# Kernel tuning notes

Hardware: AMD Instinct MI355X
Metric: run time of the kernel (lower is better)

Reference implementation:

```python
import jax, jax.numpy as jnp
import numpy as np

B, S, E, H = 2, 2048, 1024, 16
DH = E // H
SCALE = 1.0 / float(np.sqrt(E))  # note: original scales by 1/sqrt(hidden_dim), not head_dim


def _icl_mask(s):
    # triu(diagonal=0) is masked (-inf): only strictly-past positions visible,
    # except (0,0) which is explicitly unmasked so row 0 attends to itself.
    m = jnp.triu(jnp.ones((s, s), dtype=bool), k=0)
    return m.at[0, 0].set(False)


def setup_inputs() -> dict:
    key = jax.random.key(0)
    ks = jax.random.split(key, 7)
    mk = lambda k, shp: jax.random.normal(k, shp, dtype=jnp.float32)
    return {
        "q": mk(ks[0], (B, S, E)),
        "k": mk(ks[1], (B, S, E)),
        "v": mk(ks[2], (B, S, E)),
        "Wq": mk(ks[3], (E, E)) * 0.02,
        "Wk": mk(ks[4], (E, E)) * 0.02,
        "Wv": mk(ks[5], (E, E)) * 0.02,
        "Wo": mk(ks[6], (E, E)) * 0.02,
    }


def reference(q, k, v, Wq, Wk, Wv, Wo):
    b, s, e = q.shape
    h, dh = H, e // H
    # projections (nn.Linear: x @ W.T), split heads -> [b, h, s, dh]
    qh = (q @ Wq.T).reshape(b, s, h, dh).transpose(0, 2, 1, 3)
    kh = (k @ Wk.T).reshape(b, s, h, dh).transpose(0, 2, 1, 3)
    vh = (v @ Wv.T).reshape(b, s, h, dh).transpose(0, 2, 1, 3)
    scores = jnp.einsum("bhsd,bhtd->bhst", qh, kh) * SCALE  # [b,h,s,s]
    scores = jnp.where(_icl_mask(s), -jnp.inf, scores)
    probs = jax.nn.softmax(scores, axis=-1)
    out = jnp.einsum("bhst,bhtd->bhsd", probs, vh)
    out = out.transpose(0, 2, 1, 3).reshape(b, s, e)
    return out @ Wo.T
```

## Files before the change

### kernel.cpp

```cpp
#include <hip/hip_runtime.h>
#include <hip/hip_bf16.h>

typedef unsigned short u16;
typedef unsigned int u32;
typedef __bf16 bf16x8 __attribute__((ext_vector_type(8)));
typedef float float4_ __attribute__((ext_vector_type(4)));

#define B_ 2
#define S_ 2048
#define E_ 1024
#define H_ 16
#define DH_ 64
#define M_ (B_*S_)
#define E2_ (E_*E_)
#define SCALE_ 0.03125f
#define LOG2E_ 1.4426950408889634f

__device__ __forceinline__ u16 f2bf(float f) {
    unsigned int x = __float_as_uint(f);
    x += 0x7fffu + ((x >> 16) & 1u);
    return (u16)(x >> 16);
}

template <typename T> struct raw8;
template <> struct raw8<float> { float4_ lo, hi; };
template <> struct raw8<u16>   { bf16x8 v; };

__device__ __forceinline__ raw8<float> ldr8(const float* p) {
    raw8<float> r; const float4_* q = (const float4_*)p; r.lo = q[0]; r.hi = q[1]; return r;
}
__device__ __forceinline__ raw8<u16> ldr8(const u16* p) {
    raw8<u16> r; r.v = *(const bf16x8*)p; return r;
}
__device__ __forceinline__ bf16x8 cvt8(const raw8<u16>& r) { return r.v; }
__device__ __forceinline__ bf16x8 cvt8(const raw8<float>& r) {
    union { bf16x8 v; __hip_bfloat162 h[4]; } u;
    u.h[0] = __float22bfloat162_rn(float2{r.lo[0], r.lo[1]});
    u.h[1] = __float22bfloat162_rn(float2{r.lo[2], r.lo[3]});
    u.h[2] = __float22bfloat162_rn(float2{r.hi[0], r.hi[1]});
    u.h[3] = __float22bfloat162_rn(float2{r.hi[2], r.hi[3]});
    return u.v;
}
__device__ __forceinline__ bf16x8 ld8(const u16* p) { return *(const bf16x8*)p; }

__device__ __forceinline__ void async16(u16* lds, const u16* g) {
    __builtin_amdgcn_global_load_lds(
        (const __attribute__((address_space(1))) u32*)g,
        (__attribute__((address_space(3))) u32*)lds, 16, 0, 0);
}

__device__ __forceinline__ int swz32(int row, int col) {
    return row * 32 + ((((col >> 3) ^ (row & 3)) << 3) | (col & 7));
}

__global__ __launch_bounds__(256)
void convw_kernel(const float* __restrict__ Wq, const float* __restrict__ Wk,
                  const float* __restrict__ Wv, const float* __restrict__ Wo,
                  u16* __restrict__ Wqb, u16* __restrict__ Wkb,
                  u16* __restrict__ Wvb, u16* __restrict__ Wob) {
    const int which = blockIdx.y;
    const float* src = which == 0 ? Wq : which == 1 ? Wk : which == 2 ? Wv : Wo;
    u16* dst        = which == 0 ? Wqb : which == 1 ? Wkb : which == 2 ? Wvb : Wob;
    size_t off = ((size_t)blockIdx.x * 256 + threadIdx.x) * 8;
    *(bf16x8*)&dst[off] = cvt8(ldr8(&src[off]));
}

__global__ __launch_bounds__(256)
void convx_kernel(const float* __restrict__ q, const float* __restrict__ k,
                  const float* __restrict__ v,
                  u16* __restrict__ Xq, u16* __restrict__ Xk, u16* __restrict__ Xv) {
    const int which = blockIdx.y;
    const float* src = which == 0 ? q : which == 1 ? k : v;
    u16* dst        = which == 0 ? Xq : which == 1 ? Xk : Xv;
    size_t off = ((size_t)blockIdx.x * 256 + threadIdx.x) * 8;
    *(bf16x8*)&dst[off] = cvt8(ldr8(&src[off]));
}

__global__ __launch_bounds__(256)
void proj_kernel(const u16* __restrict__ Xq, const u16* __restrict__ Xk, const u16* __restrict__ Xv,
                 const u16* __restrict__ Wqb, const u16* __restrict__ Wkb, const u16* __restrict__ Wvb,
                 u16* __restrict__ Qh, u16* __restrict__ Kh, u16* __restrict__ Vt) {
    const int z = blockIdx.z;
    const u16* A   = (z == 0) ? Xq : (z == 1) ? Xk : Xv;
    const u16* Wb  = (z == 0) ? Wqb : (z == 1) ? Wkb : Wvb;
    u16* C         = (z == 0) ? Qh : (z == 1) ? Kh : Vt;
    const float cscale = (z == 0) ? SCALE_ : 1.0f;
    const int transV = (z == 2);
    const int bm = blockIdx.x * 128, bn = blockIdx.y * 128;

    __shared__ u16 As[2][128 * 32];
    __shared__ u16 Bs[2][128 * 32];

    const int tid  = threadIdx.x;
    const int lane = tid & 63;
    const int w    = tid >> 6;
    const int wr   = (w >> 1) * 64, wc = (w & 1) * 64;
    const int m16  = lane & 15, quad = lane >> 4, q4 = quad * 4;

    const int row0 = tid >> 2, ch = tid & 3, row1 = row0 + 64;
    const int csw  = ((ch ^ (row0 & 3)) * 8);
    const u16* ag0 = &A[(size_t)(bm + row0) * 1024 + csw];
    const u16* ag1 = &A[(size_t)(bm + row1) * 1024 + csw];
    const u16* wg0 = &Wb[(size_t)(bn + row0) * 1024 + csw];
    const u16* wg1 = &Wb[(size_t)(bn + row1) * 1024 + csw];

    float4_ acc[4][4];
#pragma unroll
    for (int i = 0; i < 4; i++)
#pragma unroll
        for (int j = 0; j < 4; j++) acc[i][j] = (float4_){0.f, 0.f, 0.f, 0.f};

    async16((u16*)((char*)As[0] + (size_t)tid * 16), ag0);
    async16((u16*)((char*)As[0] + (size_t)tid * 16 + 4096), ag1);
    async16((u16*)((char*)Bs[0] + (size_t)tid * 16), wg0);
    async16((u16*)((char*)Bs[0] + (size_t)tid * 16 + 4096), wg1);
    __syncthreads();

    auto step = [&](int t, const u16* Asc, const u16* Bsc, u16* Asn, u16* Bsn) {
        if (t < 31) {
            const size_t ko = (size_t)(t + 1) * 32;
            async16((u16*)((char*)Asn + (size_t)tid * 16), ag0 + ko);
            async16((u16*)((char*)Asn + (size_t)tid * 16 + 4096), ag1 + ko);
            async16((u16*)((char*)Bsn + (size_t)tid * 16), wg0 + ko);
            async16((u16*)((char*)Bsn + (size_t)tid * 16 + 4096), wg1 + ko);
        }
        __builtin_amdgcn_sched_barrier(0);
        bf16x8 af[4], bfr[4];
#pragma unroll
        for (int rt = 0; rt < 4; rt++)
            af[rt] = *(const bf16x8*)&Asc[swz32(wr + rt * 16 + m16, quad * 8)];
#pragma unroll
        for (int ct = 0; ct < 4; ct++)
            bfr[ct] = *(const bf16x8*)&Bsc[swz32(wc + ct * 16 + m16, quad * 8)];
#pragma unroll
        for (int rt = 0; rt < 4; rt++)
#pragma unroll
            for (int ct = 0; ct < 4; ct++)
                acc[rt][ct] = __builtin_amdgcn_mfma_f32_16x16x32_bf16(af[rt], bfr[ct], acc[rt][ct], 0, 0, 0);
        if (t < 31) __syncthreads();
    };

    for (int t = 0; t < 32; t += 2) {
        step(t,     As[0], Bs[0], As[1], Bs[1]);
        step(t + 1, As[1], Bs[1], As[0], Bs[0]);
    }

#pragma unroll
    for (int rt = 0; rt < 4; rt++)
#pragma unroll
        for (int ct = 0; ct < 4; ct++)
#pragma unroll
            for (int r = 0; r < 4; r++) {
                int row = bm + wr + rt * 16 + q4 + r;
                int col = bn + wc + ct * 16 + m16;
                u16 val = f2bf(acc[rt][ct][r] * cscale);
                if (!transV) {
                    C[(size_t)row * 1024 + col] = val;
                } else {
                    int bb = row >> 11, s = row & 2047;
                    C[((size_t)(bb * 1024 + col)) * 2048 + s] = val;
                }
            }
}

__global__ __launch_bounds__(256)
void out_kernel(const u16* __restrict__ AO, const u16* __restrict__ Wob, float* __restrict__ C) {
    const int bm = blockIdx.x * 128, bn = blockIdx.y * 64;

    __shared__ u16 As[2][128 * 32];
    __shared__ u16 Bs[2][64 * 32];

    const int tid  = threadIdx.x;
    const int lane = tid & 63;
    const int w    = tid >> 6;
    const int m16  = lane & 15, quad = lane >> 4, q4 = quad * 4;
    const int c1   = tid + 256;

    const int swc = (((tid & 3) ^ ((tid >> 2) & 3)) * 8);
    const u16* ag0 = &AO[(size_t)(bm + (tid >> 2)) * 1024 + swc];
    const u16* ag1 = &AO[(size_t)(bm + (c1 >> 2)) * 1024 + swc];
    const u16* bg  = &Wob[(size_t)(bn + (tid >> 2)) * 1024 + swc];

    float4_ acc[2][4];
#pragma unroll
    for (int i = 0; i < 2; i++)
#pragma unroll
        for (int j = 0; j < 4; j++) acc[i][j] = (float4_){0.f, 0.f, 0.f, 0.f};

    async16((u16*)((char*)As[0] + (size_t)tid * 16), ag0);
    async16((u16*)((char*)As[0] + (size_t)c1 * 16), ag1);
    async16((u16*)((char*)Bs[0] + (size_t)tid * 16), bg);
    __syncthreads();

    auto step = [&](int t, const u16* Asc, const u16* Bsc, u16* Asn, u16* Bsn) {
        if (t < 31) {
            async16((u16*)((char*)Asn + (size_t)tid * 16), ag0 + (t + 1) * 32);
            async16((u16*)((char*)Asn + (size_t)c1 * 16), ag1 + (t + 1) * 32);
            async16((u16*)((char*)Bsn + (size_t)tid * 16), bg + (t + 1) * 32);
        }
        __builtin_amdgcn_sched_barrier(0);
        bf16x8 af[2], bfr[4];
#pragma unroll
        for (int rt = 0; rt < 2; rt++)
            af[rt] = *(const bf16x8*)&Asc[swz32(w * 32 + rt * 16 + m16, quad * 8)];
#pragma unroll
        for (int ct = 0; ct < 4; ct++)
            bfr[ct] = *(const bf16x8*)&Bsc[swz32(ct * 16 + m16, quad * 8)];
#pragma unroll
        for (int rt = 0; rt < 2; rt++)
#pragma unroll
            for (int ct = 0; ct < 4; ct++)
                acc[rt][ct] = __builtin_amdgcn_mfma_f32_16x16x32_bf16(af[rt], bfr[ct], acc[rt][ct], 0, 0, 0);
        if (t < 31) __syncthreads();
    };

    for (int t = 0; t < 32; t += 2) {
        step(t,     As[0], Bs[0], As[1], Bs[1]);
        step(t + 1, As[1], Bs[1], As[0], Bs[0]);
    }

#pragma unroll
    for (int rt = 0; rt < 2; rt++)
#pragma unroll
        for (int ct = 0; ct < 4; ct++)
#pragma unroll
            for (int r = 0; r < 4; r++) {
                int row = bm + w * 32 + rt * 16 + q4 + r;
                int col = bn + ct * 16 + m16;
                C[(size_t)row * 1024 + col] = acc[rt][ct][r];
            }
}

__device__ __forceinline__ int sw64(int row, int col) {
    return row * 64 + ((((col >> 3) ^ (row & 7)) << 3) | (col & 7));
}

__global__ __launch_bounds__(256, 4)
void attn_kernel(const u16* __restrict__ Qh, const u16* __restrict__ Kh,
                 const u16* __restrict__ Vt, u16* __restrict__ O) {
    const int h    = blockIdx.x;
    const int tq   = 31 - blockIdx.y;
    const int b    = blockIdx.z;
    const int tid  = threadIdx.x;
    const int lane = tid & 63;
    const int w    = tid >> 6;
    const int m16  = lane & 15;
    const int quad = lane >> 4;
    const int q4   = quad * 4;

    __shared__ u16 Ks[2][64 * 64];
    __shared__ u16 Vs[2][64 * 64];
    __shared__ u16 Ps[64 * 64];

    const int srow0 = tid >> 3;
    const int srow1 = srow0 + 32;
    const int ssw   = (((tid & 7) ^ (srow0 & 7)) * 8);

    const size_t kbase = ((size_t)(b * S_)) * E_ + h * DH_;
    const size_t vbase = ((size_t)(b * 1024 + h * DH_)) * 2048;
    const u16* kg0 = &Kh[kbase + (size_t)srow0 * E_ + ssw];
    const u16* kg1 = kg0 + (size_t)32 * E_;
    const u16* vg0 = &Vt[vbase + (size_t)srow0 * 2048 + ssw];
    const u16* vg1 = vg0 + (size_t)32 * 2048;

    bf16x8 qf[2];
    {
        const u16* qa = Qh + ((size_t)(b * S_ + tq * 64 + w * 16 + m16)) * E_ + h * DH_;
        qf[0] = ld8(qa + quad * 8);
        qf[1] = ld8(qa + 32 + quad * 8);
    }

    float l_part[4] = {0.f, 0.f, 0.f, 0.f};
    float4_ o_acc[4];
#pragma unroll
    for (int dt = 0; dt < 4; dt++) o_acc[dt] = (float4_){0.f, 0.f, 0.f, 0.f};

    async16((u16*)((char*)Ks[0] + (size_t)tid * 16), kg0);
    async16((u16*)((char*)Ks[0] + (size_t)(tid + 256) * 16), kg1);
    async16((u16*)((char*)Vs[0] + (size_t)tid * 16), vg0);
    async16((u16*)((char*)Vs[0] + (size_t)(tid + 256) * 16), vg1);
    __syncthreads();

    for (int t = 0; t <= tq; t++) {
        const int buf = t & 1;
        if (t < tq) {
            const size_t ko = (size_t)(t + 1) * 64 * E_;
            const int    vo = (t + 1) * 64;
            async16((u16*)((char*)Ks[buf ^ 1] + (size_t)tid * 16), kg0 + ko);
            async16((u16*)((char*)Ks[buf ^ 1] + (size_t)(tid + 256) * 16), kg1 + ko);
            async16((u16*)((char*)Vs[buf ^ 1] + (size_t)tid * 16), vg0 + vo);
            async16((u16*)((char*)Vs[buf ^ 1] + (size_t)(tid + 256) * 16), vg1 + vo);
        }
        __builtin_amdgcn_sched_barrier(0);

        const u16* Kc = &Ks[buf][0];
        const u16* Vc = &Vs[buf][0];

        float4_ sc[4];
#pragma unroll
        for (int ct = 0; ct < 4; ct++) sc[ct] = (float4_){0.f, 0.f, 0.f, 0.f};
#pragma unroll
        for (int ks = 0; ks < 2; ks++)
#pragma unroll
            for (int ct = 0; ct < 4; ct++) {
                bf16x8 kf = *(const bf16x8*)&Kc[sw64(ct * 16 + m16, ks * 32 + quad * 8)];
                sc[ct] = __builtin_amdgcn_mfma_f32_16x16x32_bf16(qf[ks], kf, sc[ct], 0, 0, 0);
            }

        if (t != tq) {
#pragma unroll
            for (int ct = 0; ct < 4; ct++)
#pragma unroll
                for (int r = 0; r < 4; r++) {
                    float pp = exp2f(sc[ct][r] * LOG2E_);
                    l_part[r] += pp;
                    Ps[sw64(w * 16 + q4 + r, ct * 16 + m16)] = f2bf(pp);
                }
        } else {
#pragma unroll
            for (int ct = 0; ct < 4; ct++)
#pragma unroll
                for (int r = 0; r < 4; r++) {
                    int i_loc = w * 16 + q4 + r;
                    int j_loc = ct * 16 + m16;
                    bool allow = (j_loc < i_loc) || (tq == 0 && i_loc == 0 && j_loc == 0);
                    float pp = allow ? exp2f(sc[ct][r] * LOG2E_) : 0.f;
                    l_part[r] += pp;
                    Ps[sw64(w * 16 + q4 + r, ct * 16 + m16)] = f2bf(pp);
                }
        }

#pragma unroll
        for (int ks = 0; ks < 2; ks++) {
            bf16x8 pf = *(const bf16x8*)&Ps[sw64(w * 16 + m16, ks * 32 + quad * 8)];
#pragma unroll
            for (int dt = 0; dt < 4; dt++) {
                bf16x8 vf = *(const bf16x8*)&Vc[sw64(dt * 16 + m16, ks * 32 + quad * 8)];
                o_acc[dt] = __builtin_amdgcn_mfma_f32_16x16x32_bf16(pf, vf, o_acc[dt], 0, 0, 0);
            }
        }
        __syncthreads();
    }

    const size_t obase = ((size_t)(b * S_ + tq * 64)) * E_ + h * DH_;
#pragma unroll
    for (int r = 0; r < 4; r++) {
        float l = l_part[r];
#pragma unroll
        for (int msk = 1; msk <= 8; msk <<= 1) l += __shfl_xor(l, msk);
        float inv_l = 1.0f / l;
        int row = w * 16 + q4 + r;
#pragma unroll
        for (int dt = 0; dt < 4; dt++) {
            int col = dt * 16 + m16;
            O[obase + (size_t)row * E_ + col] = f2bf(o_acc[dt][r] * inv_l);
        }
    }
}

extern "C" void kernel_launch(void* const* d_in, const int* in_sizes, int n_in,
                              void* d_out, int out_size, void* d_ws, size_t ws_size,
                              hipStream_t stream) {
    const float* q  = (const float*)d_in[0];
    const float* k  = (const float*)d_in[1];
    const float* v  = (const float*)d_in[2];
    const float* Wq = (const float*)d_in[3];
    const float* Wk = (const float*)d_in[4];
    const float* Wv = (const float*)d_in[5];
    const float* Wo = (const float*)d_in[6];

    const size_t ME = (size_t)M_ * E_;
    u16* ws  = (u16*)d_ws;
    u16* Qh  = ws;
    u16* Kh  = ws + ME;
    u16* Vt  = ws + 2 * ME;
    u16* AO  = ws + 3 * ME;
    u16* Wqb = AO;
    u16* Wkb = AO + E2_;
    u16* Wvb = AO + 2 * (size_t)E2_;
    u16* Wob = ws + 4 * ME;
    u16* Xv  = ws + 4 * ME + E2_;
    u16* Xq  = (u16*)d_out;
    u16* Xk  = Xq + ME;

    dim3 blk(256);
    convw_kernel<<<dim3(512, 4), blk, 0, stream>>>(Wq, Wk, Wv, Wo, Wqb, Wkb, Wvb, Wob);
    convx_kernel<<<dim3(2048, 3), blk, 0, stream>>>(q, k, v, Xq, Xk, Xv);
    proj_kernel<<<dim3(32, 8, 3), blk, 0, stream>>>(Xq, Xk, Xv, Wqb, Wkb, Wvb, Qh, Kh, Vt);
    attn_kernel<<<dim3(16, 32, 2), blk, 0, stream>>>(Qh, Kh, Vt, AO);
    out_kernel<<<dim3(32, 16), blk, 0, stream>>>(AO, Wob, (float*)d_out);
}
```

Baseline: 218.4 us.

## Triple-buffer K/V tiles in attention with partial vmcnt waits

Moves the attention kernel's K/V staging from double to triple buffering. Loads are issued two tiles ahead, and each iteration waits with s_waitcnt vmcnt(4) plus a raw s_barrier instead of a full __syncthreads, so one tile's loads can stay in flight across the barrier. The P tile is also converted to bf16 in pairs with a packed conversion intrinsic, and launch bounds drop from 4 to 2 blocks per SM to allow for the extra LDS. The cost is more shared memory and possibly lower occupancy. The last tiles issue redundant loads of tile tq to keep the wait counts uniform.

```diff
diff --git a/kernel.cpp b/kernel.cpp
--- a/kernel.cpp
+++ b/kernel.cpp
@@ -235,7 +235,7 @@
     return row * 64 + ((((col >> 3) ^ (row & 7)) << 3) | (col & 7));
 }
 
-__global__ __launch_bounds__(256, 4)
+__global__ __launch_bounds__(256, 2)
 void attn_kernel(const u16* __restrict__ Qh, const u16* __restrict__ Kh,
                  const u16* __restrict__ Vt, u16* __restrict__ O) {
     const int h    = blockIdx.x;
@@ -248,12 +248,11 @@
     const int quad = lane >> 4;
     const int q4   = quad * 4;
 
-    __shared__ u16 Ks[2][64 * 64];
-    __shared__ u16 Vs[2][64 * 64];
+    __shared__ u16 Ks[3][64 * 64];
+    __shared__ u16 Vs[3][64 * 64];
     __shared__ u16 Ps[64 * 64];
 
     const int srow0 = tid >> 3;
-    const int srow1 = srow0 + 32;
     const int ssw   = (((tid & 7) ^ (srow0 & 7)) * 8);
 
     const size_t kbase = ((size_t)(b * S_)) * E_ + h * DH_;
@@ -275,27 +274,28 @@
 #pragma unroll
     for (int dt = 0; dt < 4; dt++) o_acc[dt] = (float4_){0.f, 0.f, 0.f, 0.f};
 
-    async16((u16*)((char*)Ks[0] + (size_t)tid * 16), kg0);
-    async16((u16*)((char*)Ks[0] + (size_t)(tid + 256) * 16), kg1);
-    async16((u16*)((char*)Vs[0] + (size_t)tid * 16), vg0);
-    async16((u16*)((char*)Vs[0] + (size_t)(tid + 256) * 16), vg1);
-    __syncthreads();
+    u16* k0 = &Ks[0][0]; u16* k1 = &Ks[1][0]; u16* k2 = &Ks[2][0];
+    u16* v0 = &Vs[0][0]; u16* v1 = &Vs[1][0]; u16* v2 = &Vs[2][0];
+
+    auto stage_to = [&](u16* kb, u16* vb, int tile) {
+        const size_t ko = (size_t)tile * 64 * E_;
+        const int    vo = tile * 64;
+        async16(kb + tid * 8, kg0 + ko);
+        async16(kb + (tid + 256) * 8, kg1 + ko);
+        async16(vb + tid * 8, vg0 + vo);
+        async16(vb + (tid + 256) * 8, vg1 + vo);
+    };
+
+    stage_to(k0, v0, 0);
+    stage_to(k1, v1, tq > 0 ? 1 : 0);
+    asm volatile("s_waitcnt vmcnt(4)" ::: "memory");
+    __builtin_amdgcn_s_barrier();
+    __builtin_amdgcn_sched_barrier(0);
 
     for (int t = 0; t <= tq; t++) {
-        const int buf = t & 1;
-        if (t < tq) {
-            const size_t ko = (size_t)(t + 1) * 64 * E_;
-            const int    vo = (t + 1) * 64;
-            async16((u16*)((char*)Ks[buf ^ 1] + (size_t)tid * 16), kg0 + ko);
-            async16((u16*)((char*)Ks[buf ^ 1] + (size_t)(tid + 256) * 16), kg1 + ko);
-            async16((u16*)((char*)Vs[buf ^ 1] + (size_t)tid * 16), vg0 + vo);
-            async16((u16*)((char*)Vs[buf ^ 1] + (size_t)(tid + 256) * 16), vg1 + vo);
-        }
+        stage_to(k2, v2, (t + 2 <= tq) ? (t + 2) : tq);
         __builtin_amdgcn_sched_barrier(0);
 
-        const u16* Kc = &Ks[buf][0];
-        const u16* Vc = &Vs[buf][0];
-
         float4_ sc[4];
 #pragma unroll
         for (int ct = 0; ct < 4; ct++) sc[ct] = (float4_){0.f, 0.f, 0.f, 0.f};
@@ -303,31 +303,36 @@
         for (int ks = 0; ks < 2; ks++)
 #pragma unroll
             for (int ct = 0; ct < 4; ct++) {
-                bf16x8 kf = *(const bf16x8*)&Kc[sw64(ct * 16 + m16, ks * 32 + quad * 8)];
+                bf16x8 kf = *(const bf16x8*)&k0[sw64(ct * 16 + m16, ks * 32 + quad * 8)];
                 sc[ct] = __builtin_amdgcn_mfma_f32_16x16x32_bf16(qf[ks], kf, sc[ct], 0, 0, 0);
             }
 
-        if (t != tq) {
-#pragma unroll
-            for (int ct = 0; ct < 4; ct++)
+#pragma unroll
+        for (int ct = 0; ct < 4; ct++) {
+            float pp[4];
+            if (t != tq) {
 #pragma unroll
                 for (int r = 0; r < 4; r++) {
-                    float pp = exp2f(sc[ct][r] * LOG2E_);
-                    l_part[r] += pp;
-                    Ps[sw64(w * 16 + q4 + r, ct * 16 + m16)] = f2bf(pp);
+                    pp[r] = exp2f(sc[ct][r] * LOG2E_);
+                    l_part[r] += pp[r];
                 }
-        } else {
-#pragma unroll
-            for (int ct = 0; ct < 4; ct++)
+            } else {
 #pragma unroll
                 for (int r = 0; r < 4; r++) {
                     int i_loc = w * 16 + q4 + r;
                     int j_loc = ct * 16 + m16;
                     bool allow = (j_loc < i_loc) || (tq == 0 && i_loc == 0 && j_loc == 0);
-                    float pp = allow ? exp2f(sc[ct][r] * LOG2E_) : 0.f;
-                    l_part[r] += pp;
-                    Ps[sw64(w * 16 + q4 + r, ct * 16 + m16)] = f2bf(pp);
+                    pp[r] = allow ? exp2f(sc[ct][r] * LOG2E_) : 0.f;
+                    l_part[r] += pp[r];
                 }
+            }
+            union { __hip_bfloat162 h; u16 s[2]; } u01, u23;
+            u01.h = __float22bfloat162_rn(float2{pp[0], pp[1]});
+            u23.h = __float22bfloat162_rn(float2{pp[2], pp[3]});
+            Ps[sw64(w * 16 + q4 + 0, ct * 16 + m16)] = u01.s[0];
+            Ps[sw64(w * 16 + q4 + 1, ct * 16 + m16)] = u01.s[1];
+            Ps[sw64(w * 16 + q4 + 2, ct * 16 + m16)] = u23.s[0];
+            Ps[sw64(w * 16 + q4 + 3, ct * 16 + m16)] = u23.s[1];
         }
 
 #pragma unroll
@@ -335,12 +340,19 @@
             bf16x8 pf = *(const bf16x8*)&Ps[sw64(w * 16 + m16, ks * 32 + quad * 8)];
 #pragma unroll
             for (int dt = 0; dt < 4; dt++) {
-                bf16x8 vf = *(const bf16x8*)&Vc[sw64(dt * 16 + m16, ks * 32 + quad * 8)];
+                bf16x8 vf = *(const bf16x8*)&v0[sw64(dt * 16 + m16, ks * 32 + quad * 8)];
                 o_acc[dt] = __builtin_amdgcn_mfma_f32_16x16x32_bf16(pf, vf, o_acc[dt], 0, 0, 0);
             }
         }
-        __syncthreads();
+
+        asm volatile("s_waitcnt vmcnt(4)" ::: "memory");
+        __builtin_amdgcn_s_barrier();
+        __builtin_amdgcn_sched_barrier(0);
+
+        u16* tk = k0; k0 = k1; k1 = k2; k2 = tk;
+        u16* tv = v0; v0 = v1; v1 = v2; v2 = tv;
     }
+    asm volatile("s_waitcnt vmcnt(0)" ::: "memory");
 
     const size_t obase = ((size_t)(b * S_ + tq * 64)) * E_ + h * DH_;
 #pragma unroll
```

Result: no change. 215.8 us (-1.2%).
